# Optimization experiments

Measured on AMD Instinct MI355X. Metric: run time of the kernel, lower is better.

## Reference

```python
import jax, jax.numpy as jnp
import numpy as np

N = 10000      # nodes
E = 320000     # edges (avg degree 32)
H = 128        # hidden_channels
G = 50         # num_gaussians
NF = 128       # num_filters
L = 6          # num_interactions
CUTOFF = 10.0


def ssp(x):
    # ShiftedSoftplus: softplus(x) - log(2)
    return jax.nn.softplus(x) - jnp.log(2.0).astype(x.dtype)


def setup_inputs() -> dict:
    key = jax.random.key(0)
    ks = jax.random.split(key, 16)
    s = 0.05
    return {
        "z": jax.random.normal(ks[0], (N, H), jnp.float32),
        "pos": jax.random.normal(ks[1], (N, 3), jnp.float32) * 3.0,
        "edge_index": jax.random.randint(ks[2], (2, E), 0, N, dtype=jnp.int64),
        # per-layer stacked parameters (PyTorch Linear convention: y = x @ W.T + b)
        "mlp1_w": jax.random.normal(ks[3], (L, NF, G), jnp.float32) * s,
        "mlp1_b": jnp.zeros((L, NF), jnp.float32),
        "mlp2_w": jax.random.normal(ks[4], (L, NF, NF), jnp.float32) * s,
        "mlp2_b": jnp.zeros((L, NF), jnp.float32),
        "lin1_w": jax.random.normal(ks[5], (L, NF, H), jnp.float32) * s,   # no bias
        "lin2_w": jax.random.normal(ks[6], (L, H, NF), jnp.float32) * s,
        "lin2_b": jnp.zeros((L, H), jnp.float32),
        "lin_w": jax.random.normal(ks[7], (L, H, H), jnp.float32) * s,
        "lin_b": jnp.zeros((L, H), jnp.float32),
        "coord_w": jax.random.normal(ks[8], (L, 1, G + 2 * H), jnp.float32) * s,
        "coord_b": jnp.zeros((L, 1), jnp.float32),
    }


def reference(z, pos, edge_index, mlp1_w, mlp1_b, mlp2_w, mlp2_b,
              lin1_w, lin2_w, lin2_b, lin_w, lin_b, coord_w, coord_b):
    row, col = edge_index[0], edge_index[1]
    # edge distances from INITIAL positions (computed once, as in torch code)
    edge_weight = jnp.linalg.norm(pos[row] - pos[col], axis=-1)          # [E]
    offset = jnp.linspace(0.0, CUTOFF, G).astype(pos.dtype)              # [G]
    coeff = -0.5 / (offset[1] - offset[0]) ** 2
    edge_attr = jnp.exp(coeff * (edge_weight[:, None] - offset[None, :]) ** 2)  # [E,G]
    C = 0.5 * (jnp.cos(edge_weight * jnp.pi / CUTOFF) + 1.0)             # [E] cosine cutoff
    ones_e = jnp.ones((E,), pos.dtype)
    h = z
    for l in range(L):
        # ---- coordinate update (uses current pos and current h) ----
        feat = jnp.concatenate([edge_attr, h[row], h[col]], axis=-1)     # [E, G+2H]
        cw = feat @ coord_w[l].T + coord_b[l]                            # [E,1]
        aggr = (pos[row] - pos[col]) * cw                                # [E,3]
        sums = jax.ops.segment_sum(aggr, row, num_segments=N)            # [N,3]
        cnt = jax.ops.segment_sum(ones_e, row, num_segments=N)           # [N]
        mean = jnp.where(cnt[:, None] > 0, sums / jnp.maximum(cnt, 1.0)[:, None], 0.0)
        pos = pos + mean
        # ---- CFConv interaction ----
        Wf = ssp(edge_attr @ mlp1_w[l].T + mlp1_b[l]) @ mlp2_w[l].T + mlp2_b[l]  # [E,NF]
        Wf = Wf * C[:, None]
        xf = h @ lin1_w[l].T                                             # [N,NF]
        agg = jax.ops.segment_sum(xf[row] * Wf, col, num_segments=N)     # [N,NF]
        out = agg @ lin2_w[l].T + lin2_b[l]                              # [N,H]
        h = h + (ssp(out) @ lin_w[l].T + lin_b[l])
    return (pos, h)
```

## Files before the change

kernel.cpp:

```cpp
#include <hip/hip_runtime.h>


#define NN 10000
#define EE 320000
#define HH 128
#define GG 50
#define NF 128
#define NL 6
#define TROWS 2048
#define NB 128

typedef unsigned short u16;
typedef unsigned int u32;
typedef short bf16x8 __attribute__((ext_vector_type(8)));
typedef float f32x4  __attribute__((ext_vector_type(4)));

__device__ __forceinline__ float us2f(u16 u){
  union { float f; u32 i; } v; v.i = ((u32)u) << 16; return v.f;
}
__device__ __forceinline__ u16 f2us(float x){
  union { float f; u32 i; } v; v.f = x;
  u32 r = v.i + 0x7fffu + ((v.i >> 16) & 1u);
  return (u16)(r >> 16);
}
__device__ __forceinline__ float ldin(const void* p, int i, int bf){
  return bf ? us2f(((const u16*)p)[i]) : ((const float*)p)[i];
}
__device__ __forceinline__ float sspf(float x){
  return fmaxf(x, 0.f) + __logf(1.f + __expf(-fabsf(x))) - 0.6931472f;
}
__device__ __forceinline__ int detect_bf(const u32* __restrict__ zraw){
  int lane = threadIdx.x & 63;
  int c = 0;
  #pragma unroll
  for(int j=0;j<4;j++){
    u32 w = zraw[lane*4+j];
    u32 hb = (w >> 8) & 0x7F;
    c += (hb >= 0x38 && hb <= 0x41) ? 1 : 0;
  }
  return __popcll(__ballot(c >= 2)) >= 32;
}
__device__ __forceinline__ int detect_i64(const int* __restrict__ ei_raw){
  int lane = threadIdx.x & 63;
  int c = 0;
  #pragma unroll
  for(int j=0;j<4;j++) c += (ei_raw[2*(lane*4+j)+1] == 0) ? 1 : 0;
  return __popcll(__ballot(c >= 3)) >= 32;
}

__global__ void k_prep(const u32* __restrict__ zraw, const void* __restrict__ pos_in,
    const void* __restrict__ mlp1_w, const void* __restrict__ mlp1_b,
    const void* __restrict__ mlp2_w, const void* __restrict__ mlp2_b,
    const void* __restrict__ lin1_w, const void* __restrict__ lin2_w,
    const void* __restrict__ lin2_b, const void* __restrict__ lin_w,
    const void* __restrict__ lin_b,  const void* __restrict__ coord_w,
    const void* __restrict__ coord_b,
    float* __restrict__ h, float* __restrict__ pc40, int* __restrict__ wmaxi,
    float* __restrict__ b1f, float* __restrict__ b2v,
    float* __restrict__ w1t, float* __restrict__ w2t,
    float* __restrict__ l1t, u16* __restrict__ l1b, u16* __restrict__ l2b,
    float* __restrict__ l2bf, u16* __restrict__ lwb,
    float* __restrict__ lbf, float* __restrict__ cwf, float* __restrict__ cbf)
{
  int bf = detect_bf(zraw);
  int b = blockIdx.x;
  if(b < NN*HH/256){
    int i = b*256 + threadIdx.x;
    h[i] = ldin(zraw, i, bf);
    if(i < NN*3){
      int n = i/3, comp = i%3;
      pc40[n*4 + comp] = ldin(pos_in, i, bf);
    }
    if(i == 0) *wmaxi = 0;
  } else {
    int i = (b - NN*HH/256)*256 + threadIdx.x;
    if(i < NL*NF){
      b1f[i]  = ldin(mlp1_b, i, bf);
      b2v[i]  = ldin(mlp2_b, i, bf);
      l2bf[i] = ldin(lin2_b, i, bf);
      lbf[i]  = ldin(lin_b,  i, bf);
    }
    if(i < NL*GG*NF){
      int l = i/(GG*NF), rem = i%(GG*NF);
      int g = rem/NF, f = rem%NF;
      w1t[i] = ldin(mlp1_w, (l*NF + f)*GG + g, bf);
    }
    if(i < NL*NF*NF){
      int l = i/(NF*NF), rem = i%(NF*NF);
      int k = rem/NF, f = rem%NF;
      w2t[i] = ldin(mlp2_w, l*NF*NF + f*NF + k, bf);
      l1t[i] = ldin(lin1_w, l*NF*HH + f*HH + k, bf);
      l1b[i] = f2us(ldin(lin1_w, i, bf));
      l2b[i] = f2us(ldin(lin2_w, i, bf));
      lwb[i] = f2us(ldin(lin_w,  i, bf));
    }
    if(i < NL*(GG+2*HH)) cwf[i] = ldin(coord_w, i, bf);
    if(i < NL) cbf[i] = ldin(coord_b, i, bf);
  }
}

__global__ void k_count(const int* __restrict__ ei_raw, const float* __restrict__ pc4,
                        int* __restrict__ eiN, float* __restrict__ wE,
                        u32* __restrict__ partR32, u32* __restrict__ partC32,
                        int* __restrict__ wmaxi){
  __shared__ u32 hr[NN/2];
  __shared__ u32 hc[NN/2];
  int is64 = detect_i64(ei_raw);
  int b = blockIdx.x, tid = threadIdx.x;
  for(int i=tid; i<NN/2; i+=256){ hr[i]=0; hc[i]=0; }
  __syncthreads();
  int e0 = b*(EE/NB), e1 = e0 + EE/NB;
  float wm = 0.f;
  for(int e = e0 + tid; e < e1; e += 256){
    int r = is64 ? ei_raw[2*e] : ei_raw[e];
    int c = is64 ? ei_raw[2*(EE+e)] : ei_raw[EE+e];
    eiN[e] = r; eiN[EE+e] = c;
    float4 pr = *(const float4*)&pc4[r*4];
    float4 pcv = *(const float4*)&pc4[c*4];
    float dx = pr.x-pcv.x, dy = pr.y-pcv.y, dz = pr.z-pcv.z;
    float w = sqrtf(dx*dx + dy*dy + dz*dz);
    wE[e] = w;
    wm = fmaxf(wm, w);
    atomicAdd(&hr[r>>1], (r&1) ? 0x10000u : 1u);
    atomicAdd(&hc[c>>1], (c&1) ? 0x10000u : 1u);
  }
  #pragma unroll
  for(int s=32; s>0; s>>=1) wm = fmaxf(wm, __shfl_down(wm, s, 64));
  if((tid & 63) == 0) atomicMax(wmaxi, __float_as_int(wm));
  __syncthreads();
  for(int i=tid; i<NN/2; i+=256){
    partR32[(size_t)b*(NN/2) + i] = hr[i];
    partC32[(size_t)b*(NN/2) + i] = hc[i];
  }
}

__global__ void k_scan2(const int* __restrict__ col_deg, const int* __restrict__ deg_row,
                        int* __restrict__ col_start, int* __restrict__ row_start){
  __shared__ int pc[1024];
  __shared__ int pr[1024];
  int tid = threadIdx.x;
  const int CH = (NN + 1023)/1024;
  int base = tid*CH;
  int sc = 0, sr = 0;
  for(int i=0;i<CH;i++){
    int idx = base+i;
    if(idx<NN){ sc += col_deg[idx]; sr += deg_row[idx]; }
  }
  pc[tid] = sc; pr[tid] = sr;
  __syncthreads();
  for(int off=1; off<1024; off<<=1){
    int vc = (tid>=off) ? pc[tid-off] : 0;
    int vr = (tid>=off) ? pr[tid-off] : 0;
    __syncthreads();
    pc[tid] += vc; pr[tid] += vr;
    __syncthreads();
  }
  int runc = (tid==0) ? 0 : pc[tid-1];
  int runr = (tid==0) ? 0 : pr[tid-1];
  for(int i=0;i<CH;i++){
    int idx = base+i;
    if(idx<NN){
      col_start[idx]=runc; runc += col_deg[idx];
      row_start[idx]=runr; runr += deg_row[idx];
    }
  }
  if(tid==1023){ col_start[NN] = runc; row_start[NN] = runr; }
}

__global__ void k_fill(const int* __restrict__ eiN, const float* __restrict__ wE,
                       const int* __restrict__ col_start, const int* __restrict__ row_start,
                       const u16* __restrict__ partR16, const u16* __restrict__ partC16,
                       int* __restrict__ row_s, float* __restrict__ wEs,
                       int* __restrict__ rcol_s, float* __restrict__ rw_s){
  __shared__ u32 hr[NN/2];
  __shared__ u32 hc[NN/2];
  int b = blockIdx.x, t = threadIdx.x;
  for(int i=t; i<NN/2; i+=256){ hr[i]=0; hc[i]=0; }
  __syncthreads();
  int e0 = b*(EE/NB), e1 = e0 + EE/NB;
  for(int e = e0 + t; e < e1; e += 256){
    int r = eiN[e], c = eiN[EE+e];
    float w = wE[e];
    u32 oldc = atomicAdd(&hc[c>>1], (c&1) ? 0x10000u : 1u);
    u32 rkc = (c&1) ? (oldc >> 16) : (oldc & 0xFFFFu);
    int p = col_start[c] + (int)partC16[(size_t)b*NN + c] + (int)rkc;
    row_s[p] = r; wEs[p] = w;
    u32 oldr = atomicAdd(&hr[r>>1], (r&1) ? 0x10000u : 1u);
    u32 rkr = (r&1) ? (oldr >> 16) : (oldr & 0xFFFFu);
    int p2 = row_start[r] + (int)partR16[(size_t)b*NN + r] + (int)rkr;
    rcol_s[p2] = c; rw_s[p2] = w;
  }
}

__global__ void k_tabnode(const float* __restrict__ w1t, const float* __restrict__ b1f,
                          const float* __restrict__ w2t, const float* __restrict__ b2v,
                          const float* __restrict__ cwf, const int* __restrict__ wmaxi,
                          u16* __restrict__ tabB, float* __restrict__ tabS,
                          const float* __restrict__ h, const float* __restrict__ l1t,
                          u16* __restrict__ xfb0, float* __restrict__ dr0,
                          float* __restrict__ pc40,
                          u16* __restrict__ partR16, u16* __restrict__ partC16,
                          int* __restrict__ degR, int* __restrict__ degC){
  __shared__ float attr[16*64];
  __shared__ float tls[128*17];
  int b = blockIdx.x, t = threadIdx.x;
  if(b < NL*128){
    int l = b >> 7;
    int r0 = (b & 127)*16;
    int f = t & 127, half = t >> 7;
    float delta = __int_as_float(*wmaxi) / (float)(TROWS-1);
    for(int idx=t; idx<16*64; idx+=256){
      int r = idx >> 6, g = idx & 63;
      float w = (float)(r0 + r)*delta;
      float d = w - (float)g*(10.f/49.f);
      attr[idx] = (g < GG) ? __expf(-12.005f*d*d) : 0.f;
    }
    __syncthreads();
    const float* __restrict__ w1 = w1t + l*GG*NF;
    float b1 = b1f[l*NF + f];
    float a1[8];
    #pragma unroll
    for(int r=0;r<8;r++) a1[r] = b1;
    for(int g=0; g<GG; g++){
      float wv = w1[g*NF + f];
      #pragma unroll
      for(int r=0;r<8;r++) a1[r] += attr[(half*8 + r)*64 + g]*wv;
    }
    #pragma unroll
    for(int r=0;r<8;r++) tls[f*17 + half*8 + r] = sspf(a1[r]);
    __syncthreads();
    const float* __restrict__ w2 = w2t + l*NF*NF;
    float b2 = b2v[l*NF + f];
    float a2[8];
    #pragma unroll
    for(int r=0;r<8;r++) a2[r] = b2;
    for(int k=0;k<NF;k++){
      float wv = w2[k*NF + f];
      #pragma unroll
      for(int r=0;r<8;r++) a2[r] += tls[k*17 + half*8 + r]*wv;
    }
    #pragma unroll
    for(int r=0;r<8;r++){
      int row = r0 + half*8 + r;
      float w = (float)row*delta;
      float C = 0.5f*(cosf(w*0.3141592653589793f) + 1.f);
      tabB[((size_t)l*TROWS + row)*NF + f] = f2us(a2[r]*C);
    }
    if(t < 16){
      const float* __restrict__ cwg = cwf + l*(GG+2*HH);
      float s = 0.f;
      for(int g=0; g<GG; g++) s += attr[t*64 + g]*cwg[g];
      tabS[l*TROWS + r0 + t] = s;
    }
  } else if(b < NL*128 + NN/8 + NN/4){
    int nb = b - NL*128;
    if(nb < NN/8){
      int f = t & 127, g = t >> 7;
      int n0 = nb*8 + g*4;
      const float* __restrict__ wt = l1t;
      float acc[4] = {0.f,0.f,0.f,0.f};
      for(int k=0;k<HH;k++){
        float wv = wt[k*NF + f];
        #pragma unroll
        for(int i=0;i<4;i++) acc[i] += h[(n0+i)*HH + k]*wv;
      }
      #pragma unroll
      for(int i=0;i<4;i++) xfb0[(n0+i)*NF + f] = f2us(acc[i]);
    } else {
      int lane = t & 63;
      int n = (nb - NN/8)*4 + (t >> 6);
      const float* __restrict__ cw = cwf;
      float h0 = h[n*HH + lane], h1 = h[n*HH + 64 + lane];
      float ar = h0*cw[GG + lane]      + h1*cw[GG + 64 + lane];
      float ac = h0*cw[GG + HH + lane] + h1*cw[GG + HH + 64 + lane];
      #pragma unroll
      for(int s=32; s>0; s>>=1){
        ar += __shfl_down(ar, s, 64);
        ac += __shfl_down(ac, s, 64);
      }
      if(lane == 0){ dr0[n] = ar; pc40[n*4+3] = ac; }
    }
  } else {
    int n = (b - (NL*128 + NN/8 + NN/4))*256 + t;
    if(n >= NN) return;
    u32 rr = 0, rc = 0;
    for(int b0=0; b0<NB; b0+=8){
      u32 vr[8], vc[8];
      #pragma unroll
      for(int j=0;j<8;j++){
        vr[j] = partR16[(size_t)(b0+j)*NN + n];
        vc[j] = partC16[(size_t)(b0+j)*NN + n];
      }
      #pragma unroll
      for(int j=0;j<8;j++){
        partR16[(size_t)(b0+j)*NN + n] = (u16)rr; rr += vr[j];
        partC16[(size_t)(b0+j)*NN + n] = (u16)rc; rc += vc[j];
      }
    }
    degR[n] = (int)rr; degC[n] = (int)rc;
  }
}

__global__ void k_layer(const int* __restrict__ col_start, const int* __restrict__ row_s,
                        const float* __restrict__ wEs, const u32* __restrict__ xfR,
                        u16* __restrict__ xfW,
                        const u16* __restrict__ tabB, const int* __restrict__ wmaxi,
                        int l,
                        const u16* __restrict__ l2b, const float* __restrict__ l2bf,
                        const u16* __restrict__ lwb, const float* __restrict__ lbf,
                        float* __restrict__ h, const u16* __restrict__ l1b,
                        const float* __restrict__ cwf,
                        const float* __restrict__ drR, float* __restrict__ drW,
                        const int* __restrict__ row_start, const int* __restrict__ rcol_s,
                        const float* __restrict__ rw_s, const float* __restrict__ tabS,
                        const float* __restrict__ cbf,
                        const float* __restrict__ pc4R, float* __restrict__ pc4W,
                        const u32* __restrict__ zraw, void* __restrict__ out){
  __shared__ __align__(16) u16 T[16*136];
  __shared__ __align__(16) u16 T2[16*136];
  int b = blockIdx.x, t = threadIdx.x;
  float invD = (float)(TROWS-1) / __int_as_float(*wmaxi);
  int wave = t >> 6, lane = t & 63;

  if(b % 3 == 0){
    int n0 = (b/3)*16;
    {
      const u32* __restrict__ tg32 = (const u32*)(tabB + (size_t)l*TROWS*NF);
      u32* __restrict__ T32 = (u32*)T;
      #pragma unroll
      for(int j=0;j<2;j++){
        int n = n0 + wave*2 + j;
        int p0 = col_start[n], p1 = col_start[n+1];
        float aa[4] = {0.f,0.f,0.f,0.f};
        float bb[4] = {0.f,0.f,0.f,0.f};
        int p = p0;
        for(; p+8 <= p1; p += 8){
          u32 gv[8], xv[8];
          #pragma unroll
          for(int k=0;k<8;k++){
            int r = row_s[p+k];
            int i0 = min((int)(wEs[p+k]*invD + 0.5f), TROWS-1);
            gv[k] = tg32[i0*64 + lane];
            xv[k] = xfR[r*64 + lane];
          }
          #pragma unroll
          for(int k=0;k<8;k++){
            aa[k&3] += us2f((u16)xv[k])      * us2f((u16)gv[k]);
            bb[k&3] += us2f((u16)(xv[k]>>16))* us2f((u16)(gv[k]>>16));
          }
        }
        for(; p < p1; p++){
          int r = row_s[p];
          int i0 = min((int)(wEs[p]*invD + 0.5f), TROWS-1);
          u32 g = tg32[i0*64 + lane];
          u32 x = xfR[r*64 + lane];
          aa[0] += us2f((u16)x)      * us2f((u16)g);
          bb[0] += us2f((u16)(x>>16))* us2f((u16)(g>>16));
        }
        float av = (aa[0]+aa[1])+(aa[2]+aa[3]);
        float bv = (bb[0]+bb[1])+(bb[2]+bb[3]);
        T32[(wave*2+j)*68 + lane] = (u32)f2us(av) | ((u32)f2us(bv) << 16);
      }
    }
    __syncthreads();
    int m16 = lane & 15, quad = lane >> 4;
    int fcol = wave*16 + m16;
    f32x4 acc;
    {
      bf16x8 aA[4];
      #pragma unroll
      for(int ks=0; ks<4; ks++)
        aA[ks] = *(const bf16x8*)&T[m16*136 + ks*32 + quad*8];
      const u16* __restrict__ wA = l2b + l*HH*NF;
      float bv = l2bf[l*HH + fcol];
      acc = (f32x4){bv,bv,bv,bv};
      #pragma unroll
      for(int ks=0; ks<4; ks++){
        bf16x8 bbv = *(const bf16x8*)&wA[fcol*NF + ks*32 + quad*8];
        acc = __builtin_amdgcn_mfma_f32_16x16x32_bf16(aA[ks], bbv, acc, 0,0,0);
      }
      #pragma unroll
      for(int r=0;r<4;r++)
        T2[(quad*4+r)*136 + fcol] = f2us(sspf(acc[r]));
    }
    __syncthreads();
    float hv[4];
    int bf = (l == NL-1) ? detect_bf(zraw) : 0;
    {
      bf16x8 aS[4];
      #pragma unroll
      for(int ks=0; ks<4; ks++)
        aS[ks] = *(const bf16x8*)&T2[m16*136 + ks*32 + quad*8];
      const u16* __restrict__ wB = lwb + l*HH*HH;
      float bv = lbf[l*HH + fcol];
      acc = (f32x4){bv,bv,bv,bv};
      #pragma unroll
      for(int ks=0; ks<4; ks++){
        bf16x8 bbv = *(const bf16x8*)&wB[fcol*HH + ks*32 + quad*8];
        acc = __builtin_amdgcn_mfma_f32_16x16x32_bf16(aS[ks], bbv, acc, 0,0,0);
      }
      #pragma unroll
      for(int r=0;r<4;r++)
        hv[r] = h[(n0+quad*4+r)*HH + fcol] + acc[r];
    }
    if(l == NL-1){
      #pragma unroll
      for(int r=0;r<4;r++){
        int n = n0 + quad*4 + r;
        if(bf) ((u16*)out)[NN*3 + n*HH + fcol] = f2us(hv[r]);
        else   ((float*)out)[NN*3 + n*HH + fcol] = hv[r];
      }
      return;
    }
    #pragma unroll
    for(int r=0;r<4;r++){
      int n = n0 + quad*4 + r;
      h[n*HH + fcol] = hv[r];
      T[(quad*4+r)*136 + fcol] = f2us(hv[r]);
    }
    __syncthreads();
    {
      bf16x8 aH[4];
      #pragma unroll
      for(int ks=0; ks<4; ks++)
        aH[ks] = *(const bf16x8*)&T[m16*136 + ks*32 + quad*8];
      const u16* __restrict__ wC = l1b + (l+1)*NF*HH;
      acc = (f32x4){0.f,0.f,0.f,0.f};
      #pragma unroll
      for(int ks=0; ks<4; ks++){
        bf16x8 bbv = *(const bf16x8*)&wC[fcol*HH + ks*32 + quad*8];
        acc = __builtin_amdgcn_mfma_f32_16x16x32_bf16(aH[ks], bbv, acc, 0,0,0);
      }
      #pragma unroll
      for(int r=0;r<4;r++)
        xfW[(n0+quad*4+r)*NF + fcol] = f2us(acc[r]);
    }
    {
      const float* __restrict__ cw = cwf + (l+1)*(GG + 2*HH);
      int j = t >> 5, l32 = t & 31;
      float ar = 0.f, ac = 0.f;
      #pragma unroll
      for(int i=0;i<4;i++){
        float hvv = us2f(T[j*136 + l32 + 32*i]);
        ar += hvv*cw[GG + l32 + 32*i];
        ac += hvv*cw[GG + HH + l32 + 32*i];
      }
      #pragma unroll
      for(int s=16; s>0; s>>=1){
        ar += __shfl_down(ar, s, 32);
        ac += __shfl_down(ac, s, 32);
      }
      if(l32 == 0){ drW[n0+j] = ar; pc4W[(n0+j)*4+3] = ac; }
    }
  } else {
    int u = b - b/3 - 1;
    int bf = (l == NL-1) ? detect_bf(zraw) : 0;
    int n = u*8 + wave;
    const float* __restrict__ ts = tabS + l*TROWS;
    float cb = cbf[l] + drR[n];
    int p0 = row_start[n], p1 = row_start[n+1];
    float4 pn = *(const float4*)&pc4R[n*4];
    float sx=0.f, sy=0.f, sz=0.f;
    for(int p = p0 + lane; p < p1; p += 64){
      int c = rcol_s[p];
      int i0 = min((int)(rw_s[p]*invD + 0.5f), TROWS-1);
      float4 pcv = *(const float4*)&pc4R[c*4];
      float a = cb + pcv.w + ts[i0];
      sx += (pn.x - pcv.x)*a;
      sy += (pn.y - pcv.y)*a;
      sz += (pn.z - pcv.z)*a;
    }
    #pragma unroll
    for(int s=32; s>0; s>>=1){
      sx += __shfl_down(sx, s, 64);
      sy += __shfl_down(sy, s, 64);
      sz += __shfl_down(sz, s, 64);
    }
    if(lane == 0){
      int cnt = p1 - p0;
      float inv = (cnt > 0) ? 1.f/(float)cnt : 0.f;
      float ox = pn.x + sx*inv, oy = pn.y + sy*inv, oz = pn.z + sz*inv;
      if(l == NL-1){
        if(bf){
          u16* o = (u16*)out;
          o[n*3+0] = f2us(ox); o[n*3+1] = f2us(oy); o[n*3+2] = f2us(oz);
        } else {
          float* o = (float*)out;
          o[n*3+0] = ox; o[n*3+1] = oy; o[n*3+2] = oz;
        }
      } else {
        pc4W[n*4+0] = ox; pc4W[n*4+1] = oy; pc4W[n*4+2] = oz;
      }
    }
  }
}

extern "C" void kernel_launch(void* const* d_in, const int* in_sizes, int n_in,
                              void* d_out, int out_size, void* d_ws, size_t ws_size,
                              hipStream_t stream){
  const u32*  z      = (const u32*)d_in[0];
  const void* pos_in = d_in[1];
  const int*  ei_raw = (const int*)d_in[2];
  const void* mlp1_w = d_in[3];
  const void* mlp1_b = d_in[4];
  const void* mlp2_w = d_in[5];
  const void* mlp2_b = d_in[6];
  const void* lin1_w = d_in[7];
  const void* lin2_w = d_in[8];
  const void* lin2_b = d_in[9];
  const void* lin_w  = d_in[10];
  const void* lin_b  = d_in[11];
  const void* coord_w= d_in[12];
  const void* coord_b= d_in[13];

  float* W = (float*)d_ws;
  float* h    = W; W += NN*HH;
  float* pc40 = W; W += NN*4;
  float* pc41 = W; W += NN*4;
  float* dr0  = W; W += NN;
  float* dr1  = W; W += NN;
  float* wE   = W; W += EE;
  float* wEs  = W; W += EE;
  float* rw_s = W; W += EE;
  float* b1f  = W; W += NL*NF;
  float* b2v  = W; W += NL*NF;
  float* w1t  = W; W += NL*GG*NF;
  float* w2t  = W; W += NL*NF*NF;
  float* l1t  = W; W += NL*NF*HH;
  float* l2bf = W; W += NL*HH;
  float* lbf  = W; W += NL*HH;
  float* cwf  = W; W += NL*(GG+2*HH);
  float* cbf  = W; W += NL;
  W = (float*)(((uintptr_t)W + 63) & ~(uintptr_t)63);
  u16*  tabB = (u16*)W; W += (size_t)NL*TROWS*NF/2;
  float* tabS = W; W += NL*TROWS;
  u16* l1b  = (u16*)W; W += (NL*NF*NF)/2;
  u16* l2b  = (u16*)W; W += (NL*NF*NF)/2;
  u16* lwb  = (u16*)W; W += (NL*NF*NF)/2;
  u16* xfb0 = (u16*)W; W += (NN*NF)/2;
  u16* xfb1 = (u16*)W; W += (NN*NF)/2;
  u16* partR16 = (u16*)W; W += (size_t)NB*NN/2;
  u16* partC16 = (u16*)W; W += (size_t)NB*NN/2;
  int* degR      = (int*)W; W += NN;
  int* degC      = (int*)W; W += NN;
  int* col_start = (int*)W; W += NN+1;
  int* row_start = (int*)W; W += NN+1;
  int* row_s     = (int*)W; W += EE;
  int* rcol_s    = (int*)W; W += EE;
  int* eiN       = (int*)W; W += 2*EE;
  int* wmaxi     = (int*)W; W += 1;

  k_prep<<<NN*HH/256 + NL*NF*NF/256, 256, 0, stream>>>(
      z, pos_in, mlp1_w, mlp1_b, mlp2_w, mlp2_b, lin1_w, lin2_w, lin2_b,
      lin_w, lin_b, coord_w, coord_b,
      h, pc40, wmaxi,
      b1f, b2v, w1t, w2t, l1t, l1b, l2b, l2bf, lwb, lbf, cwf, cbf);
  k_count<<<NB, 256, 0, stream>>>(ei_raw, pc40, eiN, wE,
                                  (u32*)partR16, (u32*)partC16, wmaxi);
  k_tabnode<<<NL*128 + NN/8 + NN/4 + (NN+255)/256, 256, 0, stream>>>(
      w1t, b1f, w2t, b2v, cwf, wmaxi, tabB, tabS,
      h, l1t, xfb0, dr0, pc40,
      partR16, partC16, degR, degC);
  k_scan2<<<1, 1024, 0, stream>>>(degC, degR, col_start, row_start);
  k_fill<<<NB, 256, 0, stream>>>(eiN, wE, col_start, row_start, partR16, partC16,
                                 row_s, wEs, rcol_s, rw_s);

  for(int l=0; l<NL; l++){
    int par = l & 1;
    const u32* xfR = (const u32*)(par ? xfb1 : xfb0);
    u16* xfW = par ? xfb0 : xfb1;
    const float* drR = par ? dr1 : dr0;   float* drW = par ? dr0 : dr1;
    const float* p4R = par ? pc41 : pc40; float* p4W = par ? pc40 : pc41;
    k_layer<<<3*(NN/16), 512, 0, stream>>>(
        col_start, row_s, wEs, xfR, xfW, tabB, wmaxi, l,
        l2b, l2bf, lwb, lbf, h, l1b, cwf,
        drR, drW,
        row_start, rcol_s, rw_s, tabS, cbf, p4R, p4W, z, d_out);
  }
}
```

Baseline: 410.9 us.

## Use bf16 MFMA for filter table and initial node projection in k_tabnode

Rewrites the filter-table build (two small MLPs over distance rows) and the initial h@lin1 projection to use bf16 MFMA 16x16x32 instructions instead of scalar fp32 FMA loops. Weights are converted to bf16 in prep, in layouts suited to MFMA operands. Rows per block double to 32, and the coordinate dot products are merged into the same node block. The goal is to cut the setup kernel's ALU time, at the cost of bf16 rounding of attr, hidden activations and h inside these setup matmuls.

```diff
diff --git a/kernel.cpp b/kernel.cpp
--- a/kernel.cpp
+++ b/kernel.cpp
@@ -57,8 +57,8 @@
     const void* __restrict__ coord_b,
     float* __restrict__ h, float* __restrict__ pc40, int* __restrict__ wmaxi,
     float* __restrict__ b1f, float* __restrict__ b2v,
-    float* __restrict__ w1t, float* __restrict__ w2t,
-    float* __restrict__ l1t, u16* __restrict__ l1b, u16* __restrict__ l2b,
+    u16* __restrict__ w1b, u16* __restrict__ w2bb,
+    u16* __restrict__ l1b, u16* __restrict__ l2b,
     float* __restrict__ l2bf, u16* __restrict__ lwb,
     float* __restrict__ lbf, float* __restrict__ cwf, float* __restrict__ cbf)
 {
@@ -80,19 +80,16 @@
       l2bf[i] = ldin(lin2_b, i, bf);
       lbf[i]  = ldin(lin_b,  i, bf);
     }
-    if(i < NL*GG*NF){
-      int l = i/(GG*NF), rem = i%(GG*NF);
-      int g = rem/NF, f = rem%NF;
-      w1t[i] = ldin(mlp1_w, (l*NF + f)*GG + g, bf);
+    if(i < NL*NF*64){
+      int l = i/(NF*64), rem = i%(NF*64);
+      int f = rem>>6, g = rem&63;
+      w1b[i] = (g < GG) ? f2us(ldin(mlp1_w, (l*NF + f)*GG + g, bf)) : (u16)0;
     }
     if(i < NL*NF*NF){
-      int l = i/(NF*NF), rem = i%(NF*NF);
-      int k = rem/NF, f = rem%NF;
-      w2t[i] = ldin(mlp2_w, l*NF*NF + f*NF + k, bf);
-      l1t[i] = ldin(lin1_w, l*NF*HH + f*HH + k, bf);
-      l1b[i] = f2us(ldin(lin1_w, i, bf));
-      l2b[i] = f2us(ldin(lin2_w, i, bf));
-      lwb[i] = f2us(ldin(lin_w,  i, bf));
+      w2bb[i] = f2us(ldin(mlp2_w, i, bf));
+      l1b[i]  = f2us(ldin(lin1_w, i, bf));
+      l2b[i]  = f2us(ldin(lin2_w, i, bf));
+      lwb[i]  = f2us(ldin(lin_w,  i, bf));
     }
     if(i < NL*(GG+2*HH)) cwf[i] = ldin(coord_w, i, bf);
     if(i < NL) cbf[i] = ldin(coord_b, i, bf);
@@ -192,96 +189,164 @@
   }
 }
 
-__global__ void k_tabnode(const float* __restrict__ w1t, const float* __restrict__ b1f,
-                          const float* __restrict__ w2t, const float* __restrict__ b2v,
+__global__ void k_tabnode(const u16* __restrict__ w1b, const float* __restrict__ b1f,
+                          const u16* __restrict__ w2bb, const float* __restrict__ b2v,
                           const float* __restrict__ cwf, const int* __restrict__ wmaxi,
                           u16* __restrict__ tabB, float* __restrict__ tabS,
-                          const float* __restrict__ h, const float* __restrict__ l1t,
+                          const float* __restrict__ h, const u16* __restrict__ l1b,
                           u16* __restrict__ xfb0, float* __restrict__ dr0,
                           float* __restrict__ pc40,
                           u16* __restrict__ partR16, u16* __restrict__ partC16,
                           int* __restrict__ degR, int* __restrict__ degC){
-  __shared__ float attr[16*64];
-  __shared__ float tls[128*17];
+  __shared__ __align__(16) u16 S[32*72 + 32*136];
   int b = blockIdx.x, t = threadIdx.x;
-  if(b < NL*128){
-    int l = b >> 7;
-    int r0 = (b & 127)*16;
-    int f = t & 127, half = t >> 7;
+  int wave = t >> 6, lane = t & 63;
+  int m16 = lane & 15, quad = lane >> 4;
+  if(b < NL*64){
+    int l = b >> 6;
+    int r0 = (b & 63)*32;
+    u16* attr = S;
+    u16* t1   = S + 32*72;
     float delta = __int_as_float(*wmaxi) / (float)(TROWS-1);
-    for(int idx=t; idx<16*64; idx+=256){
+    for(int idx=t; idx<32*64; idx+=256){
       int r = idx >> 6, g = idx & 63;
       float w = (float)(r0 + r)*delta;
       float d = w - (float)g*(10.f/49.f);
-      attr[idx] = (g < GG) ? __expf(-12.005f*d*d) : 0.f;
-    }
-    __syncthreads();
-    const float* __restrict__ w1 = w1t + l*GG*NF;
-    float b1 = b1f[l*NF + f];
-    float a1[8];
-    #pragma unroll
-    for(int r=0;r<8;r++) a1[r] = b1;
-    for(int g=0; g<GG; g++){
-      float wv = w1[g*NF + f];
-      #pragma unroll
-      for(int r=0;r<8;r++) a1[r] += attr[(half*8 + r)*64 + g]*wv;
-    }
-    #pragma unroll
-    for(int r=0;r<8;r++) tls[f*17 + half*8 + r] = sspf(a1[r]);
-    __syncthreads();
-    const float* __restrict__ w2 = w2t + l*NF*NF;
-    float b2 = b2v[l*NF + f];
-    float a2[8];
-    #pragma unroll
-    for(int r=0;r<8;r++) a2[r] = b2;
-    for(int k=0;k<NF;k++){
-      float wv = w2[k*NF + f];
-      #pragma unroll
-      for(int r=0;r<8;r++) a2[r] += tls[k*17 + half*8 + r]*wv;
-    }
-    #pragma unroll
-    for(int r=0;r<8;r++){
-      int row = r0 + half*8 + r;
-      float w = (float)row*delta;
-      float C = 0.5f*(cosf(w*0.3141592653589793f) + 1.f);
-      tabB[((size_t)l*TROWS + row)*NF + f] = f2us(a2[r]*C);
-    }
-    if(t < 16){
+      attr[r*72 + g] = (g < GG) ? f2us(__expf(-12.005f*d*d)) : (u16)0;
+    }
+    __syncthreads();
+    {
+      const u16* __restrict__ w1 = w1b + (size_t)l*NF*64;
+      f32x4 acc[2][2];
+      #pragma unroll
+      for(int nc=0;nc<2;nc++){
+        float bv = b1f[l*NF + wave*32 + nc*16 + m16];
+        #pragma unroll
+        for(int mr=0;mr<2;mr++) acc[mr][nc] = (f32x4){bv,bv,bv,bv};
+      }
+      #pragma unroll
+      for(int ks=0; ks<2; ks++){
+        bf16x8 aA[2], bB[2];
+        #pragma unroll
+        for(int mr=0;mr<2;mr++)
+          aA[mr] = *(const bf16x8*)&attr[(mr*16 + m16)*72 + ks*32 + quad*8];
+        #pragma unroll
+        for(int nc=0;nc<2;nc++)
+          bB[nc] = *(const bf16x8*)&w1[(wave*32 + nc*16 + m16)*64 + ks*32 + quad*8];
+        #pragma unroll
+        for(int mr=0;mr<2;mr++)
+          #pragma unroll
+          for(int nc=0;nc<2;nc++)
+            acc[mr][nc] = __builtin_amdgcn_mfma_f32_16x16x32_bf16(aA[mr], bB[nc], acc[mr][nc], 0,0,0);
+      }
+      #pragma unroll
+      for(int mr=0;mr<2;mr++)
+        #pragma unroll
+        for(int nc=0;nc<2;nc++)
+          #pragma unroll
+          for(int r=0;r<4;r++)
+            t1[(mr*16 + quad*4 + r)*136 + wave*32 + nc*16 + m16] = f2us(sspf(acc[mr][nc][r]));
+    }
+    __syncthreads();
+    {
+      const u16* __restrict__ w2 = w2bb + (size_t)l*NF*NF;
+      f32x4 acc[2][2];
+      #pragma unroll
+      for(int nc=0;nc<2;nc++){
+        float bv = b2v[l*NF + wave*32 + nc*16 + m16];
+        #pragma unroll
+        for(int mr=0;mr<2;mr++) acc[mr][nc] = (f32x4){bv,bv,bv,bv};
+      }
+      #pragma unroll
+      for(int ks=0; ks<4; ks++){
+        bf16x8 aA[2], bB[2];
+        #pragma unroll
+        for(int mr=0;mr<2;mr++)
+          aA[mr] = *(const bf16x8*)&t1[(mr*16 + m16)*136 + ks*32 + quad*8];
+        #pragma unroll
+        for(int nc=0;nc<2;nc++)
+          bB[nc] = *(const bf16x8*)&w2[(wave*32 + nc*16 + m16)*NF + ks*32 + quad*8];
+        #pragma unroll
+        for(int mr=0;mr<2;mr++)
+          #pragma unroll
+          for(int nc=0;nc<2;nc++)
+            acc[mr][nc] = __builtin_amdgcn_mfma_f32_16x16x32_bf16(aA[mr], bB[nc], acc[mr][nc], 0,0,0);
+      }
+      #pragma unroll
+      for(int mr=0;mr<2;mr++){
+        #pragma unroll
+        for(int r=0;r<4;r++){
+          int row = r0 + mr*16 + quad*4 + r;
+          float w = (float)row*delta;
+          float C = 0.5f*(cosf(w*0.3141592653589793f) + 1.f);
+          #pragma unroll
+          for(int nc=0;nc<2;nc++)
+            tabB[((size_t)l*TROWS + row)*NF + wave*32 + nc*16 + m16] = f2us(acc[mr][nc][r]*C);
+        }
+      }
+    }
+    if(t < 32){
       const float* __restrict__ cwg = cwf + l*(GG+2*HH);
+      float w = (float)(r0 + t)*delta;
       float s = 0.f;
-      for(int g=0; g<GG; g++) s += attr[t*64 + g]*cwg[g];
+      for(int g=0; g<GG; g++){
+        float d = w - (float)g*(10.f/49.f);
+        s += __expf(-12.005f*d*d)*cwg[g];
+      }
       tabS[l*TROWS + r0 + t] = s;
     }
-  } else if(b < NL*128 + NN/8 + NN/4){
-    int nb = b - NL*128;
-    if(nb < NN/8){
-      int f = t & 127, g = t >> 7;
-      int n0 = nb*8 + g*4;
-      const float* __restrict__ wt = l1t;
-      float acc[4] = {0.f,0.f,0.f,0.f};
-      for(int k=0;k<HH;k++){
-        float wv = wt[k*NF + f];
-        #pragma unroll
-        for(int i=0;i<4;i++) acc[i] += h[(n0+i)*HH + k]*wv;
-      }
-      #pragma unroll
-      for(int i=0;i<4;i++) xfb0[(n0+i)*NF + f] = f2us(acc[i]);
-    } else {
-      int lane = t & 63;
-      int n = (nb - NN/8)*4 + (t >> 6);
+  } else if(b < NL*64 + NN/16){
+    int n0 = (b - NL*64)*16;
+    u16* T = S;
+    {
+      int node = t >> 4, c0 = (t & 15)*8;
+      const float* hp = &h[(n0 + node)*HH + c0];
+      f32x4 v0 = *(const f32x4*)hp;
+      f32x4 v1 = *(const f32x4*)(hp+4);
+      u16* d = &T[node*136 + c0];
+      d[0]=f2us(v0[0]); d[1]=f2us(v0[1]); d[2]=f2us(v0[2]); d[3]=f2us(v0[3]);
+      d[4]=f2us(v1[0]); d[5]=f2us(v1[1]); d[6]=f2us(v1[2]); d[7]=f2us(v1[3]);
+    }
+    __syncthreads();
+    {
       const float* __restrict__ cw = cwf;
-      float h0 = h[n*HH + lane], h1 = h[n*HH + 64 + lane];
-      float ar = h0*cw[GG + lane]      + h1*cw[GG + 64 + lane];
-      float ac = h0*cw[GG + HH + lane] + h1*cw[GG + HH + 64 + lane];
-      #pragma unroll
-      for(int s=32; s>0; s>>=1){
-        ar += __shfl_down(ar, s, 64);
-        ac += __shfl_down(ac, s, 64);
-      }
-      if(lane == 0){ dr0[n] = ar; pc40[n*4+3] = ac; }
+      int j = t >> 4, l16 = t & 15;
+      float ar = 0.f, ac = 0.f;
+      #pragma unroll
+      for(int i=0;i<8;i++){
+        float hvv = us2f(T[j*136 + l16 + 16*i]);
+        ar += hvv*cw[GG + l16 + 16*i];
+        ac += hvv*cw[GG + HH + l16 + 16*i];
+      }
+      #pragma unroll
+      for(int s=8; s>0; s>>=1){
+        ar += __shfl_down(ar, s, 16);
+        ac += __shfl_down(ac, s, 16);
+      }
+      if(l16 == 0){ dr0[n0+j] = ar; pc40[(n0+j)*4+3] = ac; }
+    }
+    {
+      const u16* __restrict__ wC = l1b;
+      bf16x8 aH[4];
+      #pragma unroll
+      for(int ks=0; ks<4; ks++)
+        aH[ks] = *(const bf16x8*)&T[m16*136 + ks*32 + quad*8];
+      #pragma unroll
+      for(int nc=0; nc<2; nc++){
+        int fcol = wave*32 + nc*16 + m16;
+        f32x4 acc = (f32x4){0.f,0.f,0.f,0.f};
+        #pragma unroll
+        for(int ks=0; ks<4; ks++){
+          bf16x8 bbv = *(const bf16x8*)&wC[fcol*HH + ks*32 + quad*8];
+          acc = __builtin_amdgcn_mfma_f32_16x16x32_bf16(aH[ks], bbv, acc, 0,0,0);
+        }
+        #pragma unroll
+        for(int r=0;r<4;r++)
+          xfb0[(n0+quad*4+r)*NF + fcol] = f2us(acc[r]);
+      }
     }
   } else {
-    int n = (b - (NL*128 + NN/8 + NN/4))*256 + t;
+    int n = (b - (NL*64 + NN/16))*256 + t;
     if(n >= NN) return;
     u32 rr = 0, rc = 0;
     for(int b0=0; b0<NB; b0+=8){
@@ -524,9 +589,6 @@
   float* rw_s = W; W += EE;
   float* b1f  = W; W += NL*NF;
   float* b2v  = W; W += NL*NF;
-  float* w1t  = W; W += NL*GG*NF;
-  float* w2t  = W; W += NL*NF*NF;
-  float* l1t  = W; W += NL*NF*HH;
   float* l2bf = W; W += NL*HH;
   float* lbf  = W; W += NL*HH;
   float* cwf  = W; W += NL*(GG+2*HH);
@@ -534,6 +596,8 @@
   W = (float*)(((uintptr_t)W + 63) & ~(uintptr_t)63);
   u16*  tabB = (u16*)W; W += (size_t)NL*TROWS*NF/2;
   float* tabS = W; W += NL*TROWS;
+  u16* w1b  = (u16*)W; W += (NL*NF*64)/2;
+  u16* w2bb = (u16*)W; W += (NL*NF*NF)/2;
   u16* l1b  = (u16*)W; W += (NL*NF*NF)/2;
   u16* l2b  = (u16*)W; W += (NL*NF*NF)/2;
   u16* lwb  = (u16*)W; W += (NL*NF*NF)/2;
@@ -554,12 +618,12 @@
       z, pos_in, mlp1_w, mlp1_b, mlp2_w, mlp2_b, lin1_w, lin2_w, lin2_b,
       lin_w, lin_b, coord_w, coord_b,
       h, pc40, wmaxi,
-      b1f, b2v, w1t, w2t, l1t, l1b, l2b, l2bf, lwb, lbf, cwf, cbf);
+      b1f, b2v, w1b, w2bb, l1b, l2b, l2bf, lwb, lbf, cwf, cbf);
   k_count<<<NB, 256, 0, stream>>>(ei_raw, pc40, eiN, wE,
                                   (u32*)partR16, (u32*)partC16, wmaxi);
-  k_tabnode<<<NL*128 + NN/8 + NN/4 + (NN+255)/256, 256, 0, stream>>>(
-      w1t, b1f, w2t, b2v, cwf, wmaxi, tabB, tabS,
-      h, l1t, xfb0, dr0, pc40,
+  k_tabnode<<<NL*64 + NN/16 + (NN+255)/256, 256, 0, stream>>>(
+      w1b, b1f, w2bb, b2v, cwf, wmaxi, tabB, tabS,
+      h, l1b, xfb0, dr0, pc40,
       partR16, partC16, degR, degC);
   k_scan2<<<1, 1024, 0, stream>>>(degC, degR, col_start, row_start);
   k_fill<<<NB, 256, 0, stream>>>(eiN, wE, col_start, row_start, partR16, partC16,
```

Result: faster. 383.6 us (-6.6%).
